# Kernel optimization log

Measured on AMD Instinct MI355X. Metric: run time of the kernel, lower is better.

Reference implementation:

```python
import jax, jax.numpy as jnp
import numpy as np

D_MODEL = 1024
NUM_HEADS = 16
HEAD_DIM = D_MODEL // NUM_HEADS
SEQ_LEN = 2048
THETA = 10000.0


def setup_inputs() -> dict:
    key = jax.random.key(0)
    ks = jax.random.split(key, 9)
    s = 1.0 / np.sqrt(D_MODEL)
    inp = {
        "x": jax.random.normal(ks[0], (2, SEQ_LEN, D_MODEL), dtype=jnp.float32),
        "Wq": jax.random.uniform(ks[1], (D_MODEL, D_MODEL), jnp.float32, -s, s),
        "bq": jax.random.uniform(ks[2], (D_MODEL,), jnp.float32, -s, s),
        "Wk": jax.random.uniform(ks[3], (D_MODEL, D_MODEL), jnp.float32, -s, s),
        "bk": jax.random.uniform(ks[4], (D_MODEL,), jnp.float32, -s, s),
        "Wv": jax.random.uniform(ks[5], (D_MODEL, D_MODEL), jnp.float32, -s, s),
        "bv": jax.random.uniform(ks[6], (D_MODEL,), jnp.float32, -s, s),
        "Wo": jax.random.uniform(ks[7], (D_MODEL, D_MODEL), jnp.float32, -s, s),
        "bo": jax.random.uniform(ks[8], (D_MODEL,), jnp.float32, -s, s),
    }
    return inp


def _rope_cos_sin(seq_len, dim, theta):
    inv_freq = 1.0 / theta ** (jnp.arange(0, dim, 2, dtype=jnp.float32) / dim)  # [dim/2]
    t = jnp.arange(seq_len, dtype=jnp.float32)
    freqs = jnp.outer(t, inv_freq)  # [S, dim/2]
    return jnp.cos(freqs), jnp.sin(freqs)


def _apply_rope(x, cos, sin):
    # x: [B, H, S, head_dim]; interleaved complex pairs (even, odd)
    x2 = x.reshape(*x.shape[:-1], -1, 2)  # [B,H,S,hd/2,2]
    xe, xo = x2[..., 0], x2[..., 1]
    c = cos[None, None, :, :]
    s = sin[None, None, :, :]
    oe = xe * c - xo * s
    oo = xe * s + xo * c
    return jnp.stack([oe, oo], axis=-1).reshape(x.shape)


def reference(x, Wq, bq, Wk, bk, Wv, bv, Wo, bo):
    B, S, D = x.shape
    H, hd = NUM_HEADS, HEAD_DIM
    q = x @ Wq.T + bq
    k = x @ Wk.T + bk
    v = x @ Wv.T + bv
    # [B, H, S, hd]
    q = q.reshape(B, S, H, hd).transpose(0, 2, 1, 3)
    k = k.reshape(B, S, H, hd).transpose(0, 2, 1, 3)
    v = v.reshape(B, S, H, hd).transpose(0, 2, 1, 3)
    cos, sin = _rope_cos_sin(S, hd, THETA)
    q = _apply_rope(q, cos, sin)
    k = _apply_rope(k, cos, sin)
    scores = jnp.einsum("bhqd,bhkd->bhqk", q, k) / jnp.sqrt(jnp.float32(hd))
    causal = jnp.triu(jnp.ones((S, S), dtype=bool), k=1)
    scores = jnp.where(causal[None, None, :, :], -jnp.inf, scores)
    attn = jax.nn.softmax(scores, axis=-1)
    out = jnp.einsum("bhqk,bhkd->bhqd", attn, v)
    out = out.transpose(0, 2, 1, 3).reshape(B, S, D)
    return out @ Wo.T + bo
```

## Files before the change

### kernel.cpp

```cpp
#include <hip/hip_runtime.h>
#include <hip/hip_bf16.h>

#define S_LEN 2048
#define DM 1024
#define NH 16
#define HD 64
#define M_ROWS 4096
#define LOG2E 1.4426950408889634f
#define MASKVAL -1.0e4f
#define QSCALE 0.18033688011112042f

typedef __attribute__((ext_vector_type(8))) short short8;
typedef __attribute__((ext_vector_type(4))) float f32x4;
typedef __attribute__((ext_vector_type(16))) float f32x16;

__device__ inline ushort f2b(float f) {
  union { float f; unsigned u; } v; v.f = f;
  unsigned r = v.u + 0x7fffu + ((v.u >> 16) & 1u);
  return (ushort)(r >> 16);
}

__device__ inline float b2f(ushort u) {
  union { unsigned u; float f; } v; v.u = ((unsigned)u) << 16; return v.f;
}

__device__ inline unsigned pk_bf16(float a, float b) {
  __hip_bfloat162 h = __float22bfloat162_rn(make_float2(a, b));
  union { __hip_bfloat162 h; unsigned u; } v; v.h = h;
  return v.u;
}

__device__ inline float fexp2(float x) { return __builtin_amdgcn_exp2f(x); }

__device__ inline void gl_lds16(const void* g, void* l) {
  __builtin_amdgcn_global_load_lds(
      (const __attribute__((address_space(1))) void*)g,
      (__attribute__((address_space(3))) void*)l, 16, 0, 0);
}

__global__ __launch_bounds__(256) void cast_rope_kernel(
    const float* __restrict__ x, const float* __restrict__ Wq, const float* __restrict__ Wk,
    const float* __restrict__ Wv, const float* __restrict__ Wo,
    ushort* __restrict__ xb, ushort* __restrict__ Wqb, ushort* __restrict__ Wkb,
    ushort* __restrict__ Wvb, ushort* __restrict__ Wob,
    float* __restrict__ ropeC, float* __restrict__ ropeS) {
  const int bid = blockIdx.x;
  if (bid >= 8192) {
    int idx = (bid - 8192) * 256 + threadIdx.x;
    int s = idx >> 5, i = idx & 31;
    float inv = exp2f(-(float)i * (13.287712379549449f / 32.0f));
    float a = (float)s * inv;
    ropeC[idx] = cosf(a);
    ropeS[idx] = sinf(a);
    return;
  }
  int i = bid * 256 + threadIdx.x;
  int r = i >> 18, off = i & 0x3FFFF;
  const float4* s;
  uint2* d;
  switch (r) {
    case 0: case 1: case 2: case 3: s = (const float4*)x + i;  d = (uint2*)xb + i;  break;
    case 4: s = (const float4*)Wq + off; d = (uint2*)Wqb + off; break;
    case 5: s = (const float4*)Wk + off; d = (uint2*)Wkb + off; break;
    case 6: s = (const float4*)Wv + off; d = (uint2*)Wvb + off; break;
    default: s = (const float4*)Wo + off; d = (uint2*)Wob + off; break;
  }
  float4 v = *s;
  uint2 o;
  o.x = pk_bf16(v.x, v.y);
  o.y = pk_bf16(v.z, v.w);
  *d = o;
}

__global__ __launch_bounds__(256) void gemm_qkv_kernel(const ushort* __restrict__ xb,
    const ushort* __restrict__ Wqb, const ushort* __restrict__ Wkb, const ushort* __restrict__ Wvb,
    const float* __restrict__ bq, const float* __restrict__ bk, const float* __restrict__ bv,
    const float* __restrict__ ropeC, const float* __restrict__ ropeS,
    ushort* __restrict__ qb, ushort* __restrict__ kb, ushort* __restrict__ vT) {
  __shared__ ushort lds[17408];
  ushort* As = lds;
  ushort* Bs = lds + 8192;
  const int z = blockIdx.z;
  const ushort* W = (z == 0) ? Wqb : ((z == 1) ? Wkb : Wvb);
  const float* bias = (z == 0) ? bq : ((z == 1) ? bk : bv);
  const int m0 = blockIdx.x * 128, n0 = blockIdx.y * 128;
  const int t = threadIdx.x, lane = t & 63, wave = t >> 6;
  const int wr = (wave >> 1) * 64, wc = (wave & 1) * 64;
  const int lr = lane & 15, lg = lane >> 4;

  const int slot0 = wave * 128 + lane, slot1 = slot0 + 64;
  const int row0 = slot0 >> 2, g0 = (slot0 & 3) ^ (row0 & 3);
  const int row1 = slot1 >> 2, g1 = (slot1 & 3) ^ (row1 & 3);
  const ushort* Ap0 = &xb[(size_t)(m0 + row0) * DM + g0 * 8];
  const ushort* Ap1 = &xb[(size_t)(m0 + row1) * DM + g1 * 8];
  const ushort* Wp0 = &W[(size_t)(n0 + row0) * DM + g0 * 8];
  const ushort* Wp1 = &W[(size_t)(n0 + row1) * DM + g1 * 8];

  f32x4 acc[4][4];
#pragma unroll
  for (int a = 0; a < 4; a++)
#pragma unroll
    for (int b = 0; b < 4; b++) acc[a][b] = (f32x4){0.f, 0.f, 0.f, 0.f};

  gl_lds16(Ap0, &As[slot0 * 8]);
  gl_lds16(Ap1, &As[slot1 * 8]);
  gl_lds16(Wp0, &Bs[slot0 * 8]);
  gl_lds16(Wp1, &Bs[slot1 * 8]);
  __syncthreads();

  int buf = 0;
  for (int i = 0; i < 32; i++) {
    if (i + 1 < 32) {
      const int k0 = (i + 1) * 32;
      const int bo = (buf ^ 1) * 4096;
      gl_lds16(Ap0 + k0, &As[bo + slot0 * 8]);
      gl_lds16(Ap1 + k0, &As[bo + slot1 * 8]);
      gl_lds16(Wp0 + k0, &Bs[bo + slot0 * 8]);
      gl_lds16(Wp1 + k0, &Bs[bo + slot1 * 8]);
    }
    const int fb = buf * 4096;
    short8 af[4], bf[4];
#pragma unroll
    for (int mt = 0; mt < 4; mt++) {
      const int row = wr + mt * 16 + lr;
      af[mt] = *(const short8*)&As[fb + (row * 4 + (lg ^ (row & 3))) * 8];
    }
#pragma unroll
    for (int nt = 0; nt < 4; nt++) {
      const int row = wc + nt * 16 + lr;
      bf[nt] = *(const short8*)&Bs[fb + (row * 4 + (lg ^ (row & 3))) * 8];
    }
#pragma unroll
    for (int mt = 0; mt < 4; mt++)
#pragma unroll
      for (int nt = 0; nt < 4; nt++)
        acc[mt][nt] = __builtin_amdgcn_mfma_f32_16x16x32_bf16(af[mt], bf[nt], acc[mt][nt], 0, 0, 0);
    __syncthreads();
    buf ^= 1;
  }

#pragma unroll
  for (int mt = 0; mt < 4; mt++) {
#pragma unroll
    for (int nt = 0; nt < 4; nt++) {
      const int nloc = wc + nt * 16 + lr;
      const float bn = bias[n0 + nloc];
#pragma unroll
      for (int r = 0; r < 4; r++) {
        const int mloc = wr + mt * 16 + lg * 4 + r;
        const ushort v = f2b(acc[mt][nt][r] + bn);
        if (z < 2) lds[mloc * 136 + nloc] = v;
        else       lds[nloc * 136 + mloc] = v;
      }
    }
  }
  __syncthreads();

  const int b = m0 >> 11;
  if (z < 2) {
    ushort* dst = (z == 0) ? qb : kb;
    const float qscale = (z == 0) ? QSCALE : 1.0f;
#pragma unroll
    for (int c = 0; c < 8; c++) {
      const int sloc = c * 16 + (t >> 4);
      const int nloc = (t & 15) * 8;
      short8 val = *(const short8*)&lds[sloc * 136 + nloc];
      const int s = (m0 + sloc) & (S_LEN - 1);
      const int h = (n0 + nloc) >> 6;
      const int d0 = nloc & 63;
      const float4 cv = *(const float4*)&ropeC[s * 32 + d0 / 2];
      const float4 sv = *(const float4*)&ropeS[s * 32 + d0 / 2];
      uint4 o;
      {
        float e = b2f((ushort)val[0]), od = b2f((ushort)val[1]);
        o.x = pk_bf16((e * cv.x - od * sv.x) * qscale, (e * sv.x + od * cv.x) * qscale);
      }
      {
        float e = b2f((ushort)val[2]), od = b2f((ushort)val[3]);
        o.y = pk_bf16((e * cv.y - od * sv.y) * qscale, (e * sv.y + od * cv.y) * qscale);
      }
      {
        float e = b2f((ushort)val[4]), od = b2f((ushort)val[5]);
        o.z = pk_bf16((e * cv.z - od * sv.z) * qscale, (e * sv.z + od * cv.z) * qscale);
      }
      {
        float e = b2f((ushort)val[6]), od = b2f((ushort)val[7]);
        o.w = pk_bf16((e * cv.w - od * sv.w) * qscale, (e * sv.w + od * cv.w) * qscale);
      }
      *(uint4*)&dst[(((size_t)b * NH + h) * S_LEN + s) * HD + d0] = o;
    }
  } else {
    const int sbase = m0 & (S_LEN - 1);
#pragma unroll
    for (int c = 0; c < 8; c++) {
      const int nloc = c * 16 + (t >> 4);
      const int s0 = (t & 15) * 8;
      short8 val = *(const short8*)&lds[nloc * 136 + s0];
      const int h = (n0 + nloc) >> 6;
      const int d = nloc & 63;
      *(short8*)&vT[(((size_t)b * NH + h) * HD + d) * S_LEN + sbase + s0] = val;
    }
  }
}

__global__ __launch_bounds__(256) void flash_kernel(const ushort* __restrict__ qb,
                                                    const ushort* __restrict__ kb,
                                                    const ushort* __restrict__ vT,
                                                    ushort* __restrict__ Oh,
                                                    float* __restrict__ lsum) {
  __shared__ ushort Ks[2][4096];
  __shared__ ushort VTs[2][4096];
  const int t = threadIdx.x, lane = t & 63, wave = t >> 6;
  const int q31 = lane & 31, h = lane >> 5;
  const int bh = blockIdx.y;
  const int cid = blockIdx.x;
  const int g = (cid >= 24) ? 3 : (cid >= 12) ? 2 : (cid >= 4) ? 1 : 0;
  const int nc = g + 1;
  const int o = cid - 4 * ((g * (g + 1)) >> 1);
  const int qi = o / nc;
  const int c = o - qi * nc;
  const int qt = g * 4 + qi;
  const int q0 = qt * 128;
  const int ntiles = 2 * qt + 2;
  const int kstart = c * 8;
  const int kend = min(kstart + 8, ntiles);
  const int pidx = bh * 40 + cid;

  const ushort* kbh = kb + (size_t)bh * S_LEN * HD;
  const ushort* vbh = vT + (size_t)bh * HD * S_LEN;

  const int qrow = q0 + wave * 32 + q31;
  const ushort* qptr = qb + ((size_t)bh * S_LEN + qrow) * HD + h * 8;
  short8 qf[4];
#pragma unroll
  for (int s = 0; s < 4; s++) qf[s] = *(const short8*)(qptr + s * 16);

  const int slot0 = wave * 128 + lane, slot1 = slot0 + 64;
  const int row0 = slot0 >> 3, g0 = (slot0 & 7) ^ (row0 & 7);
  const int row1 = slot1 >> 3, g1 = (slot1 & 7) ^ (row1 & 7);
  const int lo0 = wave * 128 * 8, lo1 = lo0 + 64 * 8;

  int foff[4][2];
#pragma unroll
  for (int s = 0; s < 4; s++)
#pragma unroll
    for (int st = 0; st < 2; st++) {
      const int row = st * 32 + q31;
      foff[s][st] = (row * 8 + ((2 * s + h) ^ (row & 7))) * 8;
    }

  {
    const int k00 = kstart * 64;
    gl_lds16(kbh + (size_t)(k00 + row0) * HD + g0 * 8, &Ks[0][lo0]);
    gl_lds16(kbh + (size_t)(k00 + row1) * HD + g1 * 8, &Ks[0][lo1]);
    gl_lds16(vbh + (size_t)row0 * S_LEN + k00 + g0 * 8, &VTs[0][lo0]);
    gl_lds16(vbh + (size_t)row1 * S_LEN + k00 + g1 * 8, &VTs[0][lo1]);
  }
  __syncthreads();

  f32x16 O[2];
#pragma unroll
  for (int st = 0; st < 2; st++)
#pragma unroll
    for (int r = 0; r < 16; r++) O[st][r] = 0.f;
  float lacc = 0.f;
  int cur = 0;

  for (int kt = kstart; kt < kend; kt++) {
    if (kt + 1 < kend) {
      const int k0n = (kt + 1) * 64;
      gl_lds16(kbh + (size_t)(k0n + row0) * HD + g0 * 8, &Ks[cur ^ 1][lo0]);
      gl_lds16(kbh + (size_t)(k0n + row1) * HD + g1 * 8, &Ks[cur ^ 1][lo1]);
      gl_lds16(vbh + (size_t)row0 * S_LEN + k0n + g0 * 8, &VTs[cur ^ 1][lo0]);
      gl_lds16(vbh + (size_t)row1 * S_LEN + k0n + g1 * 8, &VTs[cur ^ 1][lo1]);
    }
    const ushort* Kb = Ks[cur];
    const ushort* Vb = VTs[cur];

    f32x16 sc[2];
#pragma unroll
    for (int st = 0; st < 2; st++)
#pragma unroll
      for (int r = 0; r < 16; r++) sc[st][r] = 0.f;
#pragma unroll
    for (int s = 0; s < 4; s++) {
#pragma unroll
      for (int st = 0; st < 2; st++) {
        const short8 kf = *(const short8*)&Kb[foff[s][st]];
        sc[st] = __builtin_amdgcn_mfma_f32_32x32x16_bf16(kf, qf[s], sc[st], 0, 0, 0);
      }
    }
    if (kt * 64 + 63 > q0 + wave * 32) {
#pragma unroll
      for (int st = 0; st < 2; st++)
#pragma unroll
        for (int r = 0; r < 16; r++) {
          const int kcol = kt * 64 + st * 32 + (r & 3) + 8 * (r >> 2) + 4 * h;
          if (kcol > qrow) sc[st][r] = MASKVAL;
        }
    }
#pragma unroll
    for (int st = 0; st < 2; st++)
#pragma unroll
      for (int r = 0; r < 16; r++) {
        const float p = fexp2(sc[st][r]);
        sc[st][r] = p;
        lacc += p;
      }

    unsigned pp[8][2];
#pragma unroll
    for (int st = 0; st < 2; st++)
#pragma unroll
      for (int rg = 0; rg < 4; rg++) {
        pp[st * 4 + rg][0] = pk_bf16(sc[st][4 * rg + 0], sc[st][4 * rg + 1]);
        pp[st * 4 + rg][1] = pk_bf16(sc[st][4 * rg + 2], sc[st][4 * rg + 3]);
      }
#pragma unroll
    for (int s = 0; s < 4; s++) {
      const unsigned sA0 = pp[2 * s][0], sA1 = pp[2 * s][1];
      const unsigned sB0 = pp[2 * s + 1][0], sB1 = pp[2 * s + 1][1];
      const unsigned send0 = h ? sA0 : sB0;
      const unsigned send1 = h ? sA1 : sB1;
      const unsigned recv0 = (unsigned)__shfl_xor((int)send0, 32);
      const unsigned recv1 = (unsigned)__shfl_xor((int)send1, 32);
      union { unsigned u[4]; short8 v; } pf;
      pf.u[0] = h ? recv0 : sA0;
      pf.u[1] = h ? recv1 : sA1;
      pf.u[2] = h ? sB0 : recv0;
      pf.u[3] = h ? sB1 : recv1;
#pragma unroll
      for (int st = 0; st < 2; st++) {
        const short8 vf = *(const short8*)&Vb[foff[s][st]];
        O[st] = __builtin_amdgcn_mfma_f32_32x32x16_bf16(vf, pf.v, O[st], 0, 0, 0);
      }
    }
    __syncthreads();
    cur ^= 1;
  }

  lacc += __shfl_xor(lacc, 32);

  ushort* obase = Oh + ((size_t)pidx * 128 + wave * 32 + q31) * HD;
#pragma unroll
  for (int st = 0; st < 2; st++)
#pragma unroll
    for (int rg = 0; rg < 4; rg++) {
      const int d0 = st * 32 + 8 * rg + 4 * h;
      uint2 w;
      w.x = pk_bf16(O[st][4 * rg + 0], O[st][4 * rg + 1]);
      w.y = pk_bf16(O[st][4 * rg + 2], O[st][4 * rg + 3]);
      *(uint2*)&obase[d0] = w;
    }
  if (h == 0) lsum[(size_t)pidx * 128 + wave * 32 + q31] = lacc;
}

__global__ __launch_bounds__(256) void combine_kernel(const ushort* __restrict__ Oh,
                                                      const float* __restrict__ lsum,
                                                      ushort* __restrict__ attn) {
  const int tid = blockIdx.x * 256 + threadIdx.x;
  const int d8 = tid & 7;
  const int q = (tid >> 3) & (S_LEN - 1);
  const int bh = tid >> 14;
  const int qt = q >> 7, row = q & 127;
  const int g = qt >> 2, nc = g + 1;
  const int base = 4 * ((g * (g + 1)) >> 1) + (qt & 3) * nc;
  const int p0 = bh * 40 + base;

  float l = 0.f;
  float acc[8];
#pragma unroll
  for (int j = 0; j < 8; j++) acc[j] = 0.f;
  for (int c = 0; c < nc; c++) {
    const size_t rowidx = (size_t)(p0 + c) * 128 + row;
    l += lsum[rowidx];
    const uint4 a = *(const uint4*)&Oh[rowidx * HD + d8 * 8];
    const unsigned au[4] = {a.x, a.y, a.z, a.w};
#pragma unroll
    for (int j = 0; j < 4; j++) {
      acc[2 * j] += b2f((ushort)(au[j] & 0xffff));
      acc[2 * j + 1] += b2f((ushort)(au[j] >> 16));
    }
  }
  const float inv = 1.f / l;
  uint4 o;
  unsigned* op = (unsigned*)&o;
#pragma unroll
  for (int j = 0; j < 4; j++) op[j] = pk_bf16(acc[2 * j] * inv, acc[2 * j + 1] * inv);
  const int b = bh >> 4, hh = bh & 15;
  *(uint4*)&attn[((size_t)b * S_LEN + q) * DM + hh * HD + d8 * 8] = o;
}

__global__ __launch_bounds__(256) void gemm_out_kernel(const ushort* __restrict__ attn,
                                                       const ushort* __restrict__ Wob,
                                                       const float* __restrict__ bo,
                                                       float* __restrict__ out) {
  __shared__ ushort As[2][4096];
  __shared__ ushort Bs[2][2048];
  const int m0 = blockIdx.x * 128, n0 = blockIdx.y * 64;
  const int t = threadIdx.x, lane = t & 63, wave = t >> 6;
  const int wm = (wave >> 1) * 64, wn = (wave & 1) * 32;
  const int lr = lane & 15, lg = lane >> 4;
  const int slotA0 = wave * 128 + lane, slotA1 = slotA0 + 64;
  const int rowA0 = slotA0 >> 2, gA0 = (slotA0 & 3) ^ (rowA0 & 3);
  const int rowA1 = slotA1 >> 2, gA1 = (slotA1 & 3) ^ (rowA1 & 3);
  const int slotB = wave * 64 + lane;
  const int rowB = slotB >> 2, gB = (slotB & 3) ^ (rowB & 3);
  const ushort* Ap0 = &attn[(size_t)(m0 + rowA0) * DM + gA0 * 8];
  const ushort* Ap1 = &attn[(size_t)(m0 + rowA1) * DM + gA1 * 8];
  const ushort* Wp  = &Wob[(size_t)(n0 + rowB) * DM + gB * 8];

  f32x4 acc[4][2];
#pragma unroll
  for (int a = 0; a < 4; a++)
#pragma unroll
    for (int b = 0; b < 2; b++) acc[a][b] = (f32x4){0.f, 0.f, 0.f, 0.f};

  gl_lds16(Ap0, &As[0][slotA0 * 8]);
  gl_lds16(Ap1, &As[0][slotA1 * 8]);
  gl_lds16(Wp, &Bs[0][slotB * 8]);
  __syncthreads();

  int buf = 0;
  for (int i = 0; i < 32; i++) {
    if (i + 1 < 32) {
      const int k0 = (i + 1) * 32;
      gl_lds16(Ap0 + k0, &As[buf ^ 1][slotA0 * 8]);
      gl_lds16(Ap1 + k0, &As[buf ^ 1][slotA1 * 8]);
      gl_lds16(Wp + k0, &Bs[buf ^ 1][slotB * 8]);
    }
    short8 af[4], bf[2];
#pragma unroll
    for (int mt = 0; mt < 4; mt++) {
      const int row = wm + mt * 16 + lr;
      af[mt] = *(const short8*)&As[buf][(row * 4 + (lg ^ (row & 3))) * 8];
    }
#pragma unroll
    for (int nt = 0; nt < 2; nt++) {
      const int row = wn + nt * 16 + lr;
      bf[nt] = *(const short8*)&Bs[buf][(row * 4 + (lg ^ (row & 3))) * 8];
    }
#pragma unroll
    for (int mt = 0; mt < 4; mt++)
#pragma unroll
      for (int nt = 0; nt < 2; nt++)
        acc[mt][nt] = __builtin_amdgcn_mfma_f32_16x16x32_bf16(af[mt], bf[nt], acc[mt][nt], 0, 0, 0);
    __syncthreads();
    buf ^= 1;
  }

#pragma unroll
  for (int mt = 0; mt < 4; mt++) {
#pragma unroll
    for (int nt = 0; nt < 2; nt++) {
      const int n = n0 + wn + nt * 16 + lr;
      const float bn = bo[n];
#pragma unroll
      for (int r = 0; r < 4; r++) {
        const int m = m0 + wm + mt * 16 + lg * 4 + r;
        out[(size_t)m * DM + n] = acc[mt][nt][r] + bn;
      }
    }
  }
}

extern "C" void kernel_launch(void* const* d_in, const int* in_sizes, int n_in,
                              void* d_out, int out_size, void* d_ws, size_t ws_size,
                              hipStream_t stream) {
  const float* x  = (const float*)d_in[0];
  const float* Wq = (const float*)d_in[1];
  const float* bq = (const float*)d_in[2];
  const float* Wk = (const float*)d_in[3];
  const float* bk = (const float*)d_in[4];
  const float* Wv = (const float*)d_in[5];
  const float* bv = (const float*)d_in[6];
  const float* Wo = (const float*)d_in[7];
  const float* bo = (const float*)d_in[8];
  float* out = (float*)d_out;

  char* ws = (char*)d_ws;
  size_t off = 0;
  auto alloc = [&](size_t bytes) { char* p = ws + off; off += (bytes + 255) & ~255ull; return p; };
  ushort* xb   = (ushort*)alloc((size_t)M_ROWS * DM * 2);
  ushort* Wqb  = (ushort*)alloc((size_t)DM * DM * 2);
  ushort* Wkb  = (ushort*)alloc((size_t)DM * DM * 2);
  ushort* Wvb  = (ushort*)alloc((size_t)DM * DM * 2);
  ushort* Wob  = (ushort*)alloc((size_t)DM * DM * 2);
  ushort* qb   = (ushort*)alloc((size_t)M_ROWS * DM * 2);
  ushort* kb   = (ushort*)alloc((size_t)M_ROWS * DM * 2);
  ushort* vTb  = (ushort*)alloc((size_t)M_ROWS * DM * 2);
  ushort* attn = (ushort*)alloc((size_t)M_ROWS * DM * 2);
  ushort* Ohb  = (ushort*)alloc((size_t)1280 * 128 * HD * 2);
  float* lsb   = (float*)alloc((size_t)1280 * 128 * 4);
  float* ropeC = (float*)alloc((size_t)S_LEN * 32 * 4);
  float* ropeS = (float*)alloc((size_t)S_LEN * 32 * 4);
  (void)ws_size; (void)in_sizes; (void)n_in; (void)out_size;

  cast_rope_kernel<<<8448, 256, 0, stream>>>(x, Wq, Wk, Wv, Wo, xb, Wqb, Wkb, Wvb, Wob,
                                             ropeC, ropeS);
  gemm_qkv_kernel<<<dim3(M_ROWS / 128, DM / 128, 3), 256, 0, stream>>>(
      xb, Wqb, Wkb, Wvb, bq, bk, bv, ropeC, ropeS, qb, kb, vTb);
  flash_kernel<<<dim3(40, 32), 256, 0, stream>>>(qb, kb, vTb, Ohb, lsb);
  combine_kernel<<<2048, 256, 0, stream>>>(Ohb, lsb, attn);
  gemm_out_kernel<<<dim3(M_ROWS / 128, DM / 64), 256, 0, stream>>>(attn, Wob, bo, out);
}
```

Baseline: 192.5 us.

## Make flash attention waves independent with tiled V layout and direct global fragment loads

Each wave now owns its own 32-row query block and key-split chunk. Work is indexed per wave (5120 units, heaviest first), so the old per-block 128-row tile is gone. K and V fragments are loaded straight from global memory into registers instead of through double-buffered LDS with __syncthreads, and V is stored in a per-64-key-tile transposed layout so those loads are contiguous. This removes block-level barriers and the causal imbalance between waves, but it drops the LDS sharing of K/V across the four waves, so global and L2 traffic per block rises and load latency is no longer hidden by prefetch.

```diff
diff --git a/kernel.cpp b/kernel.cpp
--- a/kernel.cpp
+++ b/kernel.cpp
@@ -76,7 +76,7 @@
     const ushort* __restrict__ Wqb, const ushort* __restrict__ Wkb, const ushort* __restrict__ Wvb,
     const float* __restrict__ bq, const float* __restrict__ bk, const float* __restrict__ bv,
     const float* __restrict__ ropeC, const float* __restrict__ ropeS,
-    ushort* __restrict__ qb, ushort* __restrict__ kb, ushort* __restrict__ vT) {
+    ushort* __restrict__ qb, ushort* __restrict__ kb, ushort* __restrict__ vtt) {
   __shared__ ushort lds[17408];
   ushort* As = lds;
   ushort* Bs = lds + 8192;
@@ -198,84 +198,56 @@
       short8 val = *(const short8*)&lds[nloc * 136 + s0];
       const int h = (n0 + nloc) >> 6;
       const int d = nloc & 63;
-      *(short8*)&vT[(((size_t)b * NH + h) * HD + d) * S_LEN + sbase + s0] = val;
+      const int sg = sbase + s0;
+      const int kt = sg >> 6, kin = sg & 63;
+      *(short8*)&vtt[(((size_t)(b * NH + h) * 32 + kt) * HD + d) * 64 + kin] = val;
     }
   }
 }
 
 __global__ __launch_bounds__(256) void flash_kernel(const ushort* __restrict__ qb,
                                                     const ushort* __restrict__ kb,
-                                                    const ushort* __restrict__ vT,
+                                                    const ushort* __restrict__ vtt,
                                                     ushort* __restrict__ Oh,
                                                     float* __restrict__ lsum) {
-  __shared__ ushort Ks[2][4096];
-  __shared__ ushort VTs[2][4096];
   const int t = threadIdx.x, lane = t & 63, wave = t >> 6;
   const int q31 = lane & 31, h = lane >> 5;
-  const int bh = blockIdx.y;
-  const int cid = blockIdx.x;
-  const int g = (cid >= 24) ? 3 : (cid >= 12) ? 2 : (cid >= 4) ? 1 : 0;
-  const int nc = g + 1;
-  const int o = cid - 4 * ((g * (g + 1)) >> 1);
-  const int qi = o / nc;
-  const int c = o - qi * nc;
-  const int qt = g * 4 + qi;
-  const int q0 = qt * 128;
-  const int ntiles = 2 * qt + 2;
+  const int wid = 5119 - ((int)blockIdx.x * 4 + wave);
+  const int bh = wid / 160;
+  const int u = wid - bh * 160;
+  int qb32, c, nc;
+  if (u < 16)      { nc = 1; qb32 = u;             c = 0; }
+  else if (u < 48) { nc = 2; const int r = u - 16; qb32 = 16 + (r >> 1); c = r & 1; }
+  else if (u < 96) { nc = 3; const int r = u - 48; qb32 = 32 + r / 3;    c = r - (qb32 - 32) * 3; }
+  else             { nc = 4; const int r = u - 96; qb32 = 48 + (r >> 2); c = r & 3; }
+  const int ntiles = (qb32 >> 1) + 1;
   const int kstart = c * 8;
   const int kend = min(kstart + 8, ntiles);
-  const int pidx = bh * 40 + cid;
+  const int qrow = qb32 * 32 + q31;
 
   const ushort* kbh = kb + (size_t)bh * S_LEN * HD;
-  const ushort* vbh = vT + (size_t)bh * HD * S_LEN;
-
-  const int qrow = q0 + wave * 32 + q31;
+  const ushort* vbh = vtt + (size_t)bh * 32 * HD * 64;
+
   const ushort* qptr = qb + ((size_t)bh * S_LEN + qrow) * HD + h * 8;
   short8 qf[4];
 #pragma unroll
   for (int s = 0; s < 4; s++) qf[s] = *(const short8*)(qptr + s * 16);
 
-  const int slot0 = wave * 128 + lane, slot1 = slot0 + 64;
-  const int row0 = slot0 >> 3, g0 = (slot0 & 7) ^ (row0 & 7);
-  const int row1 = slot1 >> 3, g1 = (slot1 & 7) ^ (row1 & 7);
-  const int lo0 = wave * 128 * 8, lo1 = lo0 + 64 * 8;
-
-  int foff[4][2];
-#pragma unroll
-  for (int s = 0; s < 4; s++)
-#pragma unroll
-    for (int st = 0; st < 2; st++) {
-      const int row = st * 32 + q31;
-      foff[s][st] = (row * 8 + ((2 * s + h) ^ (row & 7))) * 8;
-    }
-
-  {
-    const int k00 = kstart * 64;
-    gl_lds16(kbh + (size_t)(k00 + row0) * HD + g0 * 8, &Ks[0][lo0]);
-    gl_lds16(kbh + (size_t)(k00 + row1) * HD + g1 * 8, &Ks[0][lo1]);
-    gl_lds16(vbh + (size_t)row0 * S_LEN + k00 + g0 * 8, &VTs[0][lo0]);
-    gl_lds16(vbh + (size_t)row1 * S_LEN + k00 + g1 * 8, &VTs[0][lo1]);
-  }
-  __syncthreads();
-
   f32x16 O[2];
 #pragma unroll
   for (int st = 0; st < 2; st++)
 #pragma unroll
     for (int r = 0; r < 16; r++) O[st][r] = 0.f;
   float lacc = 0.f;
-  int cur = 0;
 
   for (int kt = kstart; kt < kend; kt++) {
-    if (kt + 1 < kend) {
-      const int k0n = (kt + 1) * 64;
-      gl_lds16(kbh + (size_t)(k0n + row0) * HD + g0 * 8, &Ks[cur ^ 1][lo0]);
-      gl_lds16(kbh + (size_t)(k0n + row1) * HD + g1 * 8, &Ks[cur ^ 1][lo1]);
-      gl_lds16(vbh + (size_t)row0 * S_LEN + k0n + g0 * 8, &VTs[cur ^ 1][lo0]);
-      gl_lds16(vbh + (size_t)row1 * S_LEN + k0n + g1 * 8, &VTs[cur ^ 1][lo1]);
-    }
-    const ushort* Kb = Ks[cur];
-    const ushort* Vb = VTs[cur];
+    const ushort* kRow = kbh + (size_t)(kt * 64 + q31) * HD + h * 8;
+    short8 kf[4][2];
+#pragma unroll
+    for (int st = 0; st < 2; st++)
+#pragma unroll
+      for (int s = 0; s < 4; s++)
+        kf[s][st] = *(const short8*)(kRow + st * 32 * HD + s * 16);
 
     f32x16 sc[2];
 #pragma unroll
@@ -283,14 +255,12 @@
 #pragma unroll
       for (int r = 0; r < 16; r++) sc[st][r] = 0.f;
 #pragma unroll
-    for (int s = 0; s < 4; s++) {
-#pragma unroll
-      for (int st = 0; st < 2; st++) {
-        const short8 kf = *(const short8*)&Kb[foff[s][st]];
-        sc[st] = __builtin_amdgcn_mfma_f32_32x32x16_bf16(kf, qf[s], sc[st], 0, 0, 0);
-      }
-    }
-    if (kt * 64 + 63 > q0 + wave * 32) {
+    for (int s = 0; s < 4; s++)
+#pragma unroll
+      for (int st = 0; st < 2; st++)
+        sc[st] = __builtin_amdgcn_mfma_f32_32x32x16_bf16(kf[s][st], qf[s], sc[st], 0, 0, 0);
+
+    if (kt == ntiles - 1) {
 #pragma unroll
       for (int st = 0; st < 2; st++)
 #pragma unroll
@@ -316,6 +286,7 @@
         pp[st * 4 + rg][0] = pk_bf16(sc[st][4 * rg + 0], sc[st][4 * rg + 1]);
         pp[st * 4 + rg][1] = pk_bf16(sc[st][4 * rg + 2], sc[st][4 * rg + 3]);
       }
+    union { unsigned u[4]; short8 v; } pf[4];
 #pragma unroll
     for (int s = 0; s < 4; s++) {
       const unsigned sA0 = pp[2 * s][0], sA1 = pp[2 * s][1];
@@ -324,24 +295,29 @@
       const unsigned send1 = h ? sA1 : sB1;
       const unsigned recv0 = (unsigned)__shfl_xor((int)send0, 32);
       const unsigned recv1 = (unsigned)__shfl_xor((int)send1, 32);
-      union { unsigned u[4]; short8 v; } pf;
-      pf.u[0] = h ? recv0 : sA0;
-      pf.u[1] = h ? recv1 : sA1;
-      pf.u[2] = h ? sB0 : recv0;
-      pf.u[3] = h ? sB1 : recv1;
-#pragma unroll
-      for (int st = 0; st < 2; st++) {
-        const short8 vf = *(const short8*)&Vb[foff[s][st]];
-        O[st] = __builtin_amdgcn_mfma_f32_32x32x16_bf16(vf, pf.v, O[st], 0, 0, 0);
-      }
-    }
-    __syncthreads();
-    cur ^= 1;
+      pf[s].u[0] = h ? recv0 : sA0;
+      pf[s].u[1] = h ? recv1 : sA1;
+      pf[s].u[2] = h ? sB0 : recv0;
+      pf[s].u[3] = h ? sB1 : recv1;
+    }
+
+    const ushort* vRow = vbh + ((size_t)kt * HD + q31) * 64 + h * 8;
+    short8 vf[4][2];
+#pragma unroll
+    for (int st = 0; st < 2; st++)
+#pragma unroll
+      for (int s = 0; s < 4; s++)
+        vf[s][st] = *(const short8*)(vRow + st * 32 * 64 + s * 16);
+#pragma unroll
+    for (int s = 0; s < 4; s++)
+#pragma unroll
+      for (int st = 0; st < 2; st++)
+        O[st] = __builtin_amdgcn_mfma_f32_32x32x16_bf16(vf[s][st], pf[s].v, O[st], 0, 0, 0);
   }
 
   lacc += __shfl_xor(lacc, 32);
 
-  ushort* obase = Oh + ((size_t)pidx * 128 + wave * 32 + q31) * HD;
+  ushort* obase = Oh + ((size_t)wid * 32 + q31) * HD;
 #pragma unroll
   for (int st = 0; st < 2; st++)
 #pragma unroll
@@ -352,7 +328,7 @@
       w.y = pk_bf16(O[st][4 * rg + 2], O[st][4 * rg + 3]);
       *(uint2*)&obase[d0] = w;
     }
-  if (h == 0) lsum[(size_t)pidx * 128 + wave * 32 + q31] = lacc;
+  if (h == 0) lsum[(size_t)wid * 32 + q31] = lacc;
 }
 
 __global__ __launch_bounds__(256) void combine_kernel(const ushort* __restrict__ Oh,
@@ -362,17 +338,17 @@
   const int d8 = tid & 7;
   const int q = (tid >> 3) & (S_LEN - 1);
   const int bh = tid >> 14;
-  const int qt = q >> 7, row = q & 127;
-  const int g = qt >> 2, nc = g + 1;
-  const int base = 4 * ((g * (g + 1)) >> 1) + (qt & 3) * nc;
-  const int p0 = bh * 40 + base;
+  const int qb32 = q >> 5, row = q & 31;
+  const int g = qb32 >> 4, nc = g + 1;
+  const int base = 16 * ((g * (g + 1)) >> 1);
+  const int p0 = bh * 160 + base + (qb32 & 15) * nc;
 
   float l = 0.f;
   float acc[8];
 #pragma unroll
   for (int j = 0; j < 8; j++) acc[j] = 0.f;
   for (int c = 0; c < nc; c++) {
-    const size_t rowidx = (size_t)(p0 + c) * 128 + row;
+    const size_t rowidx = (size_t)(p0 + c) * 32 + row;
     l += lsum[rowidx];
     const uint4 a = *(const uint4*)&Oh[rowidx * HD + d8 * 8];
     const unsigned au[4] = {a.x, a.y, a.z, a.w};
@@ -488,10 +464,10 @@
   ushort* Wob  = (ushort*)alloc((size_t)DM * DM * 2);
   ushort* qb   = (ushort*)alloc((size_t)M_ROWS * DM * 2);
   ushort* kb   = (ushort*)alloc((size_t)M_ROWS * DM * 2);
-  ushort* vTb  = (ushort*)alloc((size_t)M_ROWS * DM * 2);
+  ushort* vtt  = (ushort*)alloc((size_t)M_ROWS * DM * 2);
   ushort* attn = (ushort*)alloc((size_t)M_ROWS * DM * 2);
-  ushort* Ohb  = (ushort*)alloc((size_t)1280 * 128 * HD * 2);
-  float* lsb   = (float*)alloc((size_t)1280 * 128 * 4);
+  ushort* Ohb  = (ushort*)alloc((size_t)5120 * 32 * HD * 2);
+  float* lsb   = (float*)alloc((size_t)5120 * 32 * 4);
   float* ropeC = (float*)alloc((size_t)S_LEN * 32 * 4);
   float* ropeS = (float*)alloc((size_t)S_LEN * 32 * 4);
   (void)ws_size; (void)in_sizes; (void)n_in; (void)out_size;
@@ -499,8 +475,8 @@
   cast_rope_kernel<<<8448, 256, 0, stream>>>(x, Wq, Wk, Wv, Wo, xb, Wqb, Wkb, Wvb, Wob,
                                              ropeC, ropeS);
   gemm_qkv_kernel<<<dim3(M_ROWS / 128, DM / 128, 3), 256, 0, stream>>>(
-      xb, Wqb, Wkb, Wvb, bq, bk, bv, ropeC, ropeS, qb, kb, vTb);
-  flash_kernel<<<dim3(40, 32), 256, 0, stream>>>(qb, kb, vTb, Ohb, lsb);
+      xb, Wqb, Wkb, Wvb, bq, bk, bv, ropeC, ropeS, qb, kb, vtt);
+  flash_kernel<<<1280, 256, 0, stream>>>(qb, kb, vtt, Ohb, lsb);
   combine_kernel<<<2048, 256, 0, stream>>>(Ohb, lsb, attn);
   gemm_out_kernel<<<dim3(M_ROWS / 128, DM / 64), 256, 0, stream>>>(attn, Wob, bo, out);
 }
```

After: 236.1 us. 22.6% more time.
